# Kernel tuning notes

Measured on AMD Instinct MI355X. Metric: run time of the kernel, lower is better.

Reference implementation:

```python
import jax, jax.numpy as jnp
import numpy as np

T, N = 128, 2048
D_LIN, D_AC, D_IM = 300, 74, 35
H_LIN, H_AC, H_IM = 88, 48, 88
TOT_H = H_LIN + H_AC + H_IM          # 224
ATT_IN = 2 * TOT_H                   # 448 (window_dim=2)
MEM = 128
GAMMA_IN = ATT_IN + MEM              # 576
FINAL = TOT_H + MEM                  # 352
OUT_DIM = 1


def _lin(x, w, b):
    # torch nn.Linear: y = x @ W^T + b, W: [out, in]
    return x @ w.T + b


def _lstm_cell(x, h, c, w_ih, w_hh, b_ih, b_hh):
    # torch nn.LSTMCell gate order: i, f, g, o
    gates = x @ w_ih.T + b_ih + h @ w_hh.T + b_hh
    i, f, g, o = jnp.split(gates, 4, axis=-1)
    c2 = jax.nn.sigmoid(f) * c + jax.nn.sigmoid(i) * jnp.tanh(g)
    h2 = jax.nn.sigmoid(o) * jnp.tanh(c2)
    return h2, c2


def _forward(x_lin, x_ac, x_im, p):
    (W_ih_lin, W_hh_lin, b_ih_lin, b_hh_lin,
     W_ih_ac, W_hh_ac, b_ih_ac, b_hh_ac,
     W_ih_im, W_hh_im, b_ih_im, b_hh_im,
     att1_w1, att1_b1, att1_w2, att1_b2,
     att2_w1, att2_b1, att2_w2, att2_b2,
     g1_w1, g1_b1, g1_w2, g1_b2,
     g2_w1, g2_b1, g2_w2, g2_b2,
     out_w1, out_b1, out_w2, out_b2) = p
    n = x_lin.shape[1]
    z = lambda d: jnp.zeros((n, d), dtype=x_lin.dtype)
    init = (z(H_LIN), z(H_LIN), z(H_AC), z(H_AC), z(H_IM), z(H_IM), z(MEM))

    def step(carry, xs):
        h_l, c_l, h_a, c_a, h_i, c_i, mem = carry
        xl, xa, xi = xs
        nh_l, nc_l = _lstm_cell(xl, h_l, c_l, W_ih_lin, W_hh_lin, b_ih_lin, b_hh_lin)
        nh_a, nc_a = _lstm_cell(xa, h_a, c_a, W_ih_ac, W_hh_ac, b_ih_ac, b_hh_ac)
        nh_i, nc_i = _lstm_cell(xi, h_i, c_i, W_ih_im, W_hh_im, b_ih_im, b_hh_im)
        prev_cs = jnp.concatenate([c_l, c_a, c_i], axis=1)
        new_cs = jnp.concatenate([nc_l, nc_a, nc_i], axis=1)
        c_star = jnp.concatenate([prev_cs, new_cs], axis=1)   # [n, 448]
        attn = jax.nn.softmax(
            _lin(jax.nn.relu(_lin(c_star, att1_w1, att1_b1)), att1_w2, att1_b2), axis=1)
        attended = attn * c_star
        c_hat = jnp.tanh(
            _lin(jax.nn.relu(_lin(attended, att2_w1, att2_b1)), att2_w2, att2_b2))
        both = jnp.concatenate([attended, mem], axis=1)       # [n, 576]
        gamma1 = jax.nn.sigmoid(_lin(jax.nn.relu(_lin(both, g1_w1, g1_b1)), g1_w2, g1_b2))
        gamma2 = jax.nn.sigmoid(_lin(jax.nn.relu(_lin(both, g2_w1, g2_b1)), g2_w2, g2_b2))
        new_mem = gamma1 * mem + gamma2 * c_hat
        return ((nh_l, nc_l, nh_a, nc_a, nh_i, nc_i, new_mem),
                (nh_l, nh_a, nh_i, new_mem))

    _, (hs_l, hs_a, hs_i, mems) = jax.lax.scan(step, init, (x_lin, x_ac, x_im))
    feats = jnp.concatenate([hs_l, hs_a, hs_i, mems], axis=-1)  # [T, n, 352]
    out = _lin(jax.nn.relu(_lin(feats, out_w1, out_b1)), out_w2, out_b2)  # [T, n, 1]
    return jnp.transpose(out, (1, 0, 2))  # [n, T, 1] (torch cats over dim=1)


def setup_inputs() -> dict:
    key = jax.random.key(0)
    ks = iter(jax.random.split(key, 64))

    def rn(shape, s=0.05):
        return (jax.random.normal(next(ks), shape) * s).astype(jnp.float32)

    inp = {
        'x_linguistic': rn((T, N, D_LIN), 1.0),
        'x_acoustic': rn((T, N, D_AC), 1.0),
        'x_image': rn((T, N, D_IM), 1.0),
    }
    for name, din, h in [('lin', D_LIN, H_LIN), ('ac', D_AC, H_AC), ('im', D_IM, H_IM)]:
        inp[f'W_ih_{name}'] = rn((4 * h, din))
        inp[f'W_hh_{name}'] = rn((4 * h, h))
        inp[f'b_ih_{name}'] = rn((4 * h,))
        inp[f'b_hh_{name}'] = rn((4 * h,))
    for nm, hdim, din, dout in [('att1', 128, ATT_IN, ATT_IN),
                                ('att2', 256, ATT_IN, MEM),
                                ('g1', 64, GAMMA_IN, MEM),
                                ('g2', 64, GAMMA_IN, MEM),
                                ('out', 64, FINAL, OUT_DIM)]:
        inp[f'{nm}_w1'] = rn((hdim, din))
        inp[f'{nm}_b1'] = rn((hdim,))
        inp[f'{nm}_w2'] = rn((dout, hdim))
        inp[f'{nm}_b2'] = rn((dout,))
    return inp


def reference(x_linguistic, x_acoustic, x_image,
              W_ih_lin, W_hh_lin, b_ih_lin, b_hh_lin,
              W_ih_ac, W_hh_ac, b_ih_ac, b_hh_ac,
              W_ih_im, W_hh_im, b_ih_im, b_hh_im,
              att1_w1, att1_b1, att1_w2, att1_b2,
              att2_w1, att2_b1, att2_w2, att2_b2,
              g1_w1, g1_b1, g1_w2, g1_b2,
              g2_w1, g2_b1, g2_w2, g2_b2,
              out_w1, out_b1, out_w2, out_b2):
    p = (W_ih_lin, W_hh_lin, b_ih_lin, b_hh_lin,
         W_ih_ac, W_hh_ac, b_ih_ac, b_hh_ac,
         W_ih_im, W_hh_im, b_ih_im, b_hh_im,
         att1_w1, att1_b1, att1_w2, att1_b2,
         att2_w1, att2_b1, att2_w2, att2_b2,
         g1_w1, g1_b1, g1_w2, g1_b2,
         g2_w1, g2_b1, g2_w2, g2_b2,
         out_w1, out_b1, out_w2, out_b2)
    return _forward(x_linguistic, x_acoustic, x_image, p)
```

## Files before the change

kernel.cpp:

```cpp
#include <hip/hip_runtime.h>


#define T_STEPS 128

typedef __attribute__((ext_vector_type(8))) short bf16x8;
typedef __attribute__((ext_vector_type(4))) float f32x4;
typedef __attribute__((ext_vector_type(2))) unsigned long long ull2;

#define MFMA_B16(a,b,c) __builtin_amdgcn_mfma_f32_16x16x32_bf16((a),(b),(c),0,0,0)

__device__ __forceinline__ unsigned short f2b(float v) {
  union { float f; unsigned u; } x; x.f = v;
  unsigned r = x.u + 0x7fffu + ((x.u >> 16) & 1u);
  return (unsigned short)(r >> 16);
}
__device__ __forceinline__ float b2f(unsigned short u) {
  union { unsigned u; float f; } x; x.u = ((unsigned)u) << 16; return x.f;
}
__device__ __forceinline__ float sigm(float x){ return 1.0f/(1.0f + __expf(-x)); }
__device__ __forceinline__ float tanh_(float x){ return 1.0f - 2.0f/(1.0f + __expf(2.0f*x)); }

#define OFF_XL     0
#define OFF_XA     10496
#define OFF_XI     13824
#define OFF_CSTAR  16128
#define OFF_ATT    30720
#define OFF_HID    45312
#define OFF_G1H    53760
#define OFF_G2H    56064
#define OFF_FEATS  58368
#define OFF_BIAS   69888
#define OFF_XP     79368
#define LDS_BYTES  110344

#define BG_LIN 0
#define BG_AC  384
#define BG_IM  576
#define B_A1H  960
#define B_LOG  1088
#define B_A2H  1536
#define B_CHAT 1792
#define B_G1H  1920
#define B_G2H  1984
#define B_GM1  2048
#define B_GM2  2176
#define B_OUTH 2304
#define B_OUT2 2368
#define N_BIAS 2369

#define N_TILES 1718
#define PACK_BYTES ((size_t)N_TILES * 1024)
#define XP_ELEMS ((size_t)262144 * 960)
#define XP_BYTES (XP_ELEMS * 2)

#define LA(off,st,row,kk)  (*(const bf16x8*)(lds + (off) + ((((row)*(st)) + (kk)) << 1)))
#define LB(tile)           (*(const bf16x8*)(packc + (((size_t)(tile)) << 10) + (lane << 4)))
#define STB(off,st,row,col,v) (*(unsigned short*)(lds + (off) + ((((row)*(st)) + (col)) << 1)) = f2b(v))
#define LDB(off,st,row,col)   b2f(*(const unsigned short*)(lds + (off) + ((((row)*(st)) + (col)) << 1)))

struct PP { const float* p[35]; };

__device__ __forceinline__ void vmw(int n) {
  switch (n) {
    case 0: asm volatile("s_waitcnt vmcnt(0)"); break;
    case 1: asm volatile("s_waitcnt vmcnt(1)"); break;
    case 2: asm volatile("s_waitcnt vmcnt(2)"); break;
    case 3: asm volatile("s_waitcnt vmcnt(3)"); break;
    case 4: asm volatile("s_waitcnt vmcnt(4)"); break;
    case 5: asm volatile("s_waitcnt vmcnt(5)"); break;
    case 6: asm volatile("s_waitcnt vmcnt(6)"); break;
    default: asm volatile("s_waitcnt vmcnt(7)"); break;
  }
  __builtin_amdgcn_sched_barrier(0);
}

#define ISSUE_B(dst, tile)                                                   \
  { unsigned off_ = (((unsigned)(tile)) << 10) + ((unsigned)lane << 4);      \
    asm volatile("global_load_dwordx4 %0, %1, %2"                            \
                 : "=v"(dst) : "v"(off_), "s"(packc)); }

template<int NTT, class FT, class FB>
__device__ __forceinline__ void reg_loop(const char* packc, int lane,
                                         FT&& tile_of, FB&& body)
{
  constexpr int D = (NTT < 8) ? NTT : 8;
  bf16x8 b[8];
  #pragma unroll
  for (int i = 0; i < D; ++i) ISSUE_B(b[i], tile_of(i));
  #pragma unroll
  for (int i = 0; i < NTT; ++i) {
    vmw((NTT-1-i) < 7 ? (NTT-1-i) : 7);
    body(i, b[i & 7]);
    __builtin_amdgcn_sched_barrier(0);
    if (i + 8 < NTT) ISSUE_B(b[i & 7], tile_of(i + 8));
  }
}

__device__ __forceinline__ float gate_src(const float* Wih, const float* Whh,
                                          int H, int din, int nksx, int col, int k)
{
  int blk = col >> 6, gate = (col >> 4) & 3, u = col & 15;
  int unit = blk*16 + u;
  if (unit >= H) return 0.f;
  int row = gate*H + unit;
  int xk = nksx*32;
  if (k < xk) return (k < din) ? Wih[row*din + k] : 0.f;
  int kk = k - xk;
  return (kk < H) ? Whh[row*H + kk] : 0.f;
}
__device__ __forceinline__ float gate_h(const float* Whh, int H, int col, int k)
{
  int blk = col >> 6, gate = (col >> 4) & 3, u = col & 15;
  int unit = blk*16 + u;
  if (unit >= H || k >= H) return 0.f;
  return Whh[(gate*H + unit)*H + k];
}
__device__ __forceinline__ float gate_x(const float* Wih, int H, int din, int col, int k)
{
  int blk = col >> 6, gate = (col >> 4) & 3, u = col & 15;
  int unit = blk*16 + u;
  if (unit >= H || k >= din) return 0.f;
  return Wih[(gate*H + unit)*din + k];
}
__device__ __forceinline__ float plain_src(const float* W, int nout, int kdim, int col, int k)
{
  return (col < nout && k < kdim) ? W[col*kdim + k] : 0.f;
}

__global__ __launch_bounds__(256) void pack_kernel(PP P, unsigned short* __restrict__ pack,
                                                   float* __restrict__ bias)
{
  int tid = blockIdx.x*blockDim.x + threadIdx.x;
  int wv = tid >> 6, lane = tid & 63;
  int nw = (gridDim.x*blockDim.x) >> 6;
  int c = lane & 15, kg = lane >> 4;

  for (int tile = wv; tile < N_TILES; tile += nw) {
    unsigned short* dst = pack + ((size_t)tile << 9) + lane*8;
    #pragma unroll
    for (int i = 0; i < 8; ++i) {
      int r = tile; int nt, ks; float v; int kk;
      if (r < 312)       { nt=r/13; ks=r-nt*13; kk=ks*32+kg*8+i; v = gate_src(P.p[3], P.p[4], 88,300,10, nt*16+c, kk); }
      else if (r < 372)  { r-=312; nt=r/5;  ks=r-nt*5;  kk=ks*32+kg*8+i; v = gate_src(P.p[7], P.p[8], 48, 74, 3, nt*16+c, kk); }
      else if (r < 492)  { r-=372; nt=r/5;  ks=r-nt*5;  kk=ks*32+kg*8+i; v = gate_src(P.p[11],P.p[12],88, 35, 2, nt*16+c, kk); }
      else if (r < 604)  { r-=492; nt=r/14; ks=r-nt*14; kk=ks*32+kg*8+i; v = plain_src(P.p[15],128,448, nt*16+c, kk); }
      else if (r < 716)  { r-=604; nt=r/4;  ks=r-nt*4;  kk=ks*32+kg*8+i; v = plain_src(P.p[17],448,128, nt*16+c, kk); }
      else if (r < 940)  { r-=716; nt=r/14; ks=r-nt*14; kk=ks*32+kg*8+i; v = plain_src(P.p[19],256,448, nt*16+c, kk); }
      else if (r < 1004) { r-=940; nt=r/8;  ks=r-nt*8;  kk=ks*32+kg*8+i; v = plain_src(P.p[21],128,256, nt*16+c, kk); }
      else if (r < 1076) { r-=1004; nt=r/18; ks=r-nt*18; kk=ks*32+kg*8+i; v = plain_src(P.p[23], 64,576, nt*16+c, kk); }
      else if (r < 1148) { r-=1076; nt=r/18; ks=r-nt*18; kk=ks*32+kg*8+i; v = plain_src(P.p[27], 64,576, nt*16+c, kk); }
      else if (r < 1164) { r-=1148; nt=r/2;  ks=r-nt*2;  kk=ks*32+kg*8+i; v = plain_src(P.p[25],128, 64, nt*16+c, kk); }
      else if (r < 1180) { r-=1164; nt=r/2;  ks=r-nt*2;  kk=ks*32+kg*8+i; v = plain_src(P.p[29],128, 64, nt*16+c, kk); }
      else if (r < 1224) { r-=1180; nt=r/11; ks=r-nt*11; kk=ks*32+kg*8+i; v = plain_src(P.p[31], 64,352, nt*16+c, kk); }
      else if (r < 1226) { r-=1224; ks=r;    kk=ks*32+kg*8+i; v = plain_src(P.p[33],  1, 64, c, kk); }
      else if (r < 1298) { r-=1226; nt=r/3;  ks=r-nt*3;  kk=ks*32+kg*8+i; v = gate_h(P.p[4], 88, nt*16+c, kk); }
      else if (r < 1322) { r-=1298; nt=r/2;  ks=r-nt*2;  kk=ks*32+kg*8+i; v = gate_h(P.p[8], 48, nt*16+c, kk); }
      else if (r < 1394) { r-=1322; nt=r/3;  ks=r-nt*3;  kk=ks*32+kg*8+i; v = gate_h(P.p[12],88, nt*16+c, kk); }
      else if (r < 1634) { r-=1394; nt=r/10; ks=r-nt*10; kk=ks*32+kg*8+i; v = gate_x(P.p[3], 88,300, nt*16+c, kk); }
      else if (r < 1670) { r-=1634; nt=r/3;  ks=r-nt*3;  kk=ks*32+kg*8+i; v = gate_x(P.p[7], 48, 74, nt*16+c, kk); }
      else               { r-=1670; nt=r/2;  ks=r-nt*2;  kk=ks*32+kg*8+i; v = gate_x(P.p[11],88, 35, nt*16+c, kk); }
      dst[i] = f2b(v);
    }
  }

  int NT = gridDim.x*blockDim.x;
  for (int b = tid; b < N_BIAS; b += NT) {
    float v; int r = b;
    if (r < 384)       { int blk=r>>6, g=(r>>4)&3, u=r&15, un=blk*16+u; v = (un<88) ? P.p[5][g*88+un] + P.p[6][g*88+un]  : 0.f; }
    else if (r < 576)  { r-=384; int blk=r>>6, g=(r>>4)&3, u=r&15, un=blk*16+u; v = (un<48) ? P.p[9][g*48+un] + P.p[10][g*48+un] : 0.f; }
    else if (r < 960)  { r-=576; int blk=r>>6, g=(r>>4)&3, u=r&15, un=blk*16+u; v = (un<88) ? P.p[13][g*88+un]+ P.p[14][g*88+un] : 0.f; }
    else if (r < 1088) v = P.p[16][r-960];
    else if (r < 1536) v = P.p[18][r-1088];
    else if (r < 1792) v = P.p[20][r-1536];
    else if (r < 1920) v = P.p[22][r-1792];
    else if (r < 1984) v = P.p[24][r-1920];
    else if (r < 2048) v = P.p[28][r-1984];
    else if (r < 2176) v = P.p[26][r-2048];
    else if (r < 2304) v = P.p[30][r-2176];
    else if (r < 2368) v = P.p[32][r-2304];
    else               v = P.p[34][0];
    bias[b] = v;
  }
}

__global__ __launch_bounds__(1024) void xproj_kernel(
    const float* __restrict__ xlin, const float* __restrict__ xac,
    const float* __restrict__ xim, const unsigned short* __restrict__ pack,
    unsigned short* __restrict__ xp)
{
  __shared__ alignas(16) char slds[81920];
  const char* packc = (const char*)pack;
  const int tid = threadIdx.x, lane = tid & 63, w = tid >> 6;
  const int rA = lane & 15, gA = lane >> 4;
  const int mt = w & 7, half = w >> 3;
  const size_t m0 = (size_t)blockIdx.x * 128;
  const int mr = mt * 16;

  for (int p = tid; p < 9600; p += 1024) {
    int row = p/75, d = p - row*75;
    float4 v = *(const float4*)(xlin + (m0+row)*300 + d*4);
    unsigned long long u = (unsigned long long)f2b(v.x)
      | ((unsigned long long)f2b(v.y) << 16)
      | ((unsigned long long)f2b(v.z) << 32)
      | ((unsigned long long)f2b(v.w) << 48);
    *(unsigned long long*)(slds + (((size_t)row*320 + d*4) << 1)) = u;
  }
  for (int p = tid; p < 1280; p += 1024) {
    int row = p/10, cc = 300 + 2*(p - row*10);
    *(unsigned*)(slds + (((size_t)row*320 + cc) << 1)) = 0;
  }
  __syncthreads();
  for (int blk = half*3; blk < half*3 + 3; ++blk) {
    #pragma unroll
    for (int q = 0; q < 4; ++q) {
      f32x4 acc = {0.f,0.f,0.f,0.f};
      int nt = blk*4 + q;
      bf16x8 a = *(const bf16x8*)(slds + ((((mr+rA)*320) + gA*8) << 1));
      reg_loop<10>(packc, lane,
        [&](int i){ return 1394 + nt*10 + i; },
        [&](int i, bf16x8 bv){
          acc = MFMA_B16(a, bv, acc);
          if (i + 1 < 10) a = *(const bf16x8*)(slds + ((((mr+rA)*320) + (i+1)*32 + gA*8) << 1));
        });
      #pragma unroll
      for (int j = 0; j < 4; ++j)
        xp[(m0 + mr + gA*4 + j)*960 + blk*64 + q*16 + rA] = f2b(acc[j]);
    }
  }
  __syncthreads();

  for (int p = tid; p < 4736; p += 1024) {
    int row = p/37, d = p - row*37;
    float2 v = *(const float2*)(xac + (m0+row)*74 + d*2);
    unsigned uu = (unsigned)f2b(v.x) | ((unsigned)f2b(v.y) << 16);
    *(unsigned*)(slds + (((size_t)row*96 + d*2) << 1)) = uu;
  }
  for (int p = tid; p < 1408; p += 1024) {
    int row = p/11, cc = 74 + 2*(p - row*11);
    *(unsigned*)(slds + (((size_t)row*96 + cc) << 1)) = 0;
  }
  __syncthreads();
  if (half == 0) {
    for (int blk = 0; blk < 3; ++blk) {
      #pragma unroll
      for (int q = 0; q < 4; ++q) {
        f32x4 acc = {0.f,0.f,0.f,0.f};
        int nt = blk*4 + q;
        bf16x8 a = *(const bf16x8*)(slds + ((((mr+rA)*96) + gA*8) << 1));
        reg_loop<3>(packc, lane,
          [&](int i){ return 1634 + nt*3 + i; },
          [&](int i, bf16x8 bv){
            acc = MFMA_B16(a, bv, acc);
            if (i + 1 < 3) a = *(const bf16x8*)(slds + ((((mr+rA)*96) + (i+1)*32 + gA*8) << 1));
          });
        #pragma unroll
        for (int j = 0; j < 4; ++j)
          xp[(m0 + mr + gA*4 + j)*960 + 384 + blk*64 + q*16 + rA] = f2b(acc[j]);
      }
    }
  }
  __syncthreads();

  for (int p = tid; p < 4480; p += 1024) {
    int row = p/35, d = p - row*35;
    *(unsigned short*)(slds + (((size_t)row*64 + d) << 1)) = f2b(xim[(m0+row)*35 + d]);
  }
  for (int p = tid; p < 3712; p += 1024) {
    int row = p/29, cc = 35 + (p - row*29);
    *(unsigned short*)(slds + (((size_t)row*64 + cc) << 1)) = 0;
  }
  __syncthreads();
  if (half == 1) {
    for (int blk = 0; blk < 6; ++blk) {
      #pragma unroll
      for (int q = 0; q < 4; ++q) {
        f32x4 acc = {0.f,0.f,0.f,0.f};
        int nt = blk*4 + q;
        bf16x8 a = *(const bf16x8*)(slds + ((((mr+rA)*64) + gA*8) << 1));
        reg_loop<2>(packc, lane,
          [&](int i){ return 1670 + nt*2 + i; },
          [&](int i, bf16x8 bv){
            acc = MFMA_B16(a, bv, acc);
            if (i + 1 < 2) a = *(const bf16x8*)(slds + ((((mr+rA)*64) + 32 + gA*8) << 1));
          });
        #pragma unroll
        for (int j = 0; j < 4; ++j)
          xp[(m0 + mr + gA*4 + j)*960 + 576 + blk*64 + q*16 + rA] = f2b(acc[j]);
      }
    }
  }
}

struct GT { int blk, tb, kt, nksx, nks, xoff, xst, hsec, bb, H; };
__device__ __forceinline__ GT gate_task(int tau) {
  GT g;
  if (tau < 6)       { g.blk=tau;   g.tb=0   + g.blk*4*13; g.kt=13; g.nksx=10; g.nks=13; g.xoff=OFF_XL; g.xst=328; g.hsec=0;   g.bb=BG_LIN; g.H=88; }
  else if (tau < 9)  { g.blk=tau-6; g.tb=312 + g.blk*4*5;  g.kt=5;  g.nksx=3;  g.nks=5;  g.xoff=OFF_XA; g.xst=104; g.hsec=88;  g.bb=BG_AC;  g.H=48; }
  else               { g.blk=tau-9; g.tb=372 + g.blk*4*5;  g.kt=5;  g.nksx=2;  g.nks=5;  g.xoff=OFF_XI; g.xst=72;  g.hsec=136; g.bb=BG_IM;  g.H=88; }
  return g;
}

template<int NKSX,int NKS>
__device__ __forceinline__ void gate_reg(f32x4 acc[4], const char* lds, const char* packc,
    int lane, int rA, int gA, int xoff, int xst, int hsec, int tb, int kt)
{
  bf16x8 a = LA(xoff, xst, rA, gA*8);
  reg_loop<NKS*4>(packc, lane,
    [&](int i){ return tb + (i & 3)*kt + (i >> 2); },
    [&](int i, bf16x8 bv){
      int q = i & 3, s = i >> 2;
      acc[q] = MFMA_B16(a, bv, acc[q]);
      if (q == 3 && s + 1 < NKS) {
        int s2 = s + 1;
        a = (s2 < NKSX) ? LA(xoff, xst, rA, s2*32 + gA*8)
                        : LA(OFF_FEATS, 360, rA, hsec + (s2-NKSX)*32 + gA*8);
      }
    });
}

template<int NKS>
__device__ __forceinline__ void gate_reg_h(f32x4 acc[4], const char* lds, const char* packc,
    int lane, int rA, int gA, int hsec, int tb)
{
  bf16x8 a = LA(OFF_FEATS, 360, rA, hsec + gA*8);
  reg_loop<NKS*4>(packc, lane,
    [&](int i){ return tb + (i & 3)*NKS + (i >> 2); },
    [&](int i, bf16x8 bv){
      int q = i & 3, s = i >> 2;
      acc[q] = MFMA_B16(a, bv, acc[q]);
      if (q == 3 && s + 1 < NKS)
        a = LA(OFF_FEATS, 360, rA, hsec + (s+1)*32 + gA*8);
    });
}

__device__ __forceinline__ void stage_x(char* lds, const float* __restrict__ xlin,
    const float* __restrict__ xac, const float* __restrict__ xim, int t, int n0,
    int tid0, int nthr)
{
  const size_t tb = (size_t)t*2048 + n0;
  for (int q = tid0; q < 1200; q += nthr) {
    int row = q/75, d = q - row*75;
    float4 v = *(const float4*)(xlin + (tb+row)*300 + d*4);
    unsigned long long u = (unsigned long long)f2b(v.x)
      | ((unsigned long long)f2b(v.y) << 16)
      | ((unsigned long long)f2b(v.z) << 32)
      | ((unsigned long long)f2b(v.w) << 48);
    *(unsigned long long*)(lds + OFF_XL + (((size_t)row*328 + d*4) << 1)) = u;
  }
  for (int q = tid0; q < 592; q += nthr) {
    int row = q/37, d = q - row*37;
    float2 v = *(const float2*)(xac + (tb+row)*74 + d*2);
    unsigned uu = (unsigned)f2b(v.x) | ((unsigned)f2b(v.y) << 16);
    *(unsigned*)(lds + OFF_XA + (((size_t)row*104 + d*2) << 1)) = uu;
  }
  for (int q = tid0; q < 560; q += nthr) {
    int row = q/35, d = q - row*35;
    *(unsigned short*)(lds + OFF_XI + (((size_t)row*72 + d) << 1)) = f2b(xim[(tb+row)*35 + d]);
  }
}

__device__ __forceinline__ void stage_xp(char* lds, const unsigned short* __restrict__ xp,
                                         int t, int n0, int tid0, int nthr)
{
  const size_t base = ((size_t)t*2048 + n0)*960;
  for (int q = tid0; q < 1920; q += nthr) {
    int row = q/120, ch = q - row*120;
    ull2 v = *(const ull2*)(xp + base + (size_t)row*960 + ch*8);
    *(ull2*)(lds + OFF_XP + (((size_t)row*968 + ch*8) << 1)) = v;
  }
}

template<int XPATH>
__global__ __launch_bounds__(1024) void fused_kernel(
    const float* __restrict__ xlin, const float* __restrict__ xac, const float* __restrict__ xim,
    const unsigned short* __restrict__ pack, const float* __restrict__ biasg,
    const unsigned short* __restrict__ xp, float* __restrict__ out)
{
  __shared__ alignas(16) char lds[LDS_BYTES];
  const char* packc = (const char*)pack;
  const int tid  = threadIdx.x;
  const int lane = tid & 63;
  const int w    = tid >> 6;
  const int rA   = lane & 15;
  const int gA   = lane >> 4;
  const int n0   = blockIdx.x * 16;
  float* biasLds = (float*)(lds + OFF_BIAS);

  for (int i = tid; i < (OFF_BIAS >> 2); i += 1024) ((int*)lds)[i] = 0;
  __syncthreads();
  for (int i = tid; i < N_BIAS; i += 1024) biasLds[i] = biasg[i];
  if (XPATH) stage_xp(lds, xp, 0, n0, tid, 1024);
  else       stage_x(lds, xlin, xac, xim, 0, n0, tid, 1024);
  __syncthreads();

  float cst[4]  = {};
  float mreg[4] = {};

  for (int t = 0; t < T_STEPS; ++t) {
    f32x4 gacc[4];
    if (w == 15) {
      if (t > 0) {
        float bv = biasLds[B_OUT2];
        f32x4 oa0 = {bv,bv,bv,bv};
        bf16x8 as[2], bs[2];
        #pragma unroll
        for (int s = 0; s < 2; ++s) { bs[s] = LB(1224 + s); as[s] = LA(OFF_HID,72, rA, s*32+gA*8); }
        #pragma unroll
        for (int s = 0; s < 2; ++s) oa0 = MFMA_B16(as[s], bs[s], oa0);
        if (rA == 0) {
          #pragma unroll
          for (int j = 0; j < 4; ++j)
            __builtin_nontemporal_store(oa0[j], &out[(size_t)(n0 + gA*4 + j)*T_STEPS + (t-1)]);
        }
      }
    } else if (XPATH) {
      int blk, tb, nks, hsec, bb, cb;
      if (w < 6)      { blk=w;   tb=1226+w*12;      nks=3; hsec=0;   bb=BG_LIN; cb=0   + w*64; }
      else if (w < 9) { blk=w-6; tb=1298+(w-6)*8;   nks=2; hsec=88;  bb=BG_AC;  cb=384 + (w-6)*64; }
      else            { blk=w-9; tb=1322+(w-9)*12;  nks=3; hsec=136; bb=BG_IM;  cb=576 + (w-9)*64; }
      #pragma unroll
      for (int q = 0; q < 4; ++q) {
        float bv = biasLds[bb + blk*64 + q*16 + rA];
        #pragma unroll
        for (int j = 0; j < 4; ++j) {
          int row = gA*4 + j;
          float xv = b2f(*(const unsigned short*)(lds + OFF_XP + (((size_t)row*968 + cb + q*16 + rA) << 1)));
          gacc[q][j] = bv + xv;
        }
      }
      if (nks == 3) gate_reg_h<3>(gacc, lds, packc, lane, rA, gA, hsec, tb);
      else          gate_reg_h<2>(gacc, lds, packc, lane, rA, gA, hsec, tb);
    } else {
      GT g = gate_task(w);
      #pragma unroll
      for (int q = 0; q < 4; ++q) {
        float bv = biasLds[g.bb + g.blk*64 + q*16 + rA];
        gacc[q] = (f32x4){bv,bv,bv,bv};
      }
      if (w < 6)      gate_reg<10,13>(gacc, lds, packc, lane, rA, gA, g.xoff, g.xst, g.hsec, g.tb, g.kt);
      else if (w < 9) gate_reg<3,5>  (gacc, lds, packc, lane, rA, gA, g.xoff, g.xst, g.hsec, g.tb, g.kt);
      else            gate_reg<2,5>  (gacc, lds, packc, lane, rA, gA, g.xoff, g.xst, g.hsec, g.tb, g.kt);
    }
    __syncthreads();

    if (w < 15) {
      GT g = gate_task(w);
      int unit = g.blk*16 + rA;
      if (unit < g.H) {
        #pragma unroll
        for (int j = 0; j < 4; ++j) {
          float iv = sigm (gacc[0][j]);
          float fv = sigm (gacc[1][j]);
          float gv = tanh_(gacc[2][j]);
          float ov = sigm (gacc[3][j]);
          float cp = cst[j];
          float cn = fv*cp + iv*gv;
          float hn = ov*tanh_(cn);
          cst[j] = cn;
          int row = gA*4 + j;
          STB(OFF_CSTAR,456, row, g.hsec + unit,        cp);
          STB(OFF_CSTAR,456, row, 224 + g.hsec + unit,  cn);
          STB(OFF_FEATS,360, row, g.hsec + unit,        hn);
        }
      }
    }
    __syncthreads();

    if (w < 8) {
      int n = w;
      float bv = biasLds[B_A1H + n*16 + rA];
      f32x4 a0v = {bv,bv,bv,bv};
      bf16x8 a = LA(OFF_CSTAR,456, rA, gA*8);
      reg_loop<14>(packc, lane,
        [&](int i){ return 492 + n*14 + i; },
        [&](int i, bf16x8 bv8){
          a0v = MFMA_B16(a, bv8, a0v);
          if (i + 1 < 14) a = LA(OFF_CSTAR,456, rA, (i+1)*32+gA*8);
        });
      #pragma unroll
      for (int j = 0; j < 4; ++j)
        STB(OFF_HID,136, gA*4 + j, n*16 + rA, fmaxf(a0v[j], 0.f));
    }
    __syncthreads();

    {
      float bv1 = biasLds[B_LOG + w*16 + rA];
      if (w < 12) {
        float bv2 = biasLds[B_LOG + (w+16)*16 + rA];
        f32x4 l0 = {bv1,bv1,bv1,bv1}, l1 = {bv2,bv2,bv2,bv2};
        bf16x8 a = LA(OFF_HID,136, rA, gA*8);
        reg_loop<8>(packc, lane,
          [&](int i){ int tau = (i < 4) ? w : (w + 16); return 604 + tau*4 + (i & 3); },
          [&](int i, bf16x8 bv8){
            if (i < 4) l0 = MFMA_B16(a, bv8, l0); else l1 = MFMA_B16(a, bv8, l1);
            if (i + 1 < 8) a = LA(OFF_HID,136, rA, ((i+1)&3)*32+gA*8);
          });
        #pragma unroll
        for (int j = 0; j < 4; ++j) {
          STB(OFF_ATT,456, gA*4 + j, w*16 + rA,      l0[j]);
          STB(OFF_ATT,456, gA*4 + j, (w+16)*16 + rA, l1[j]);
        }
      } else {
        f32x4 l0 = {bv1,bv1,bv1,bv1};
        bf16x8 a = LA(OFF_HID,136, rA, gA*8);
        reg_loop<4>(packc, lane,
          [&](int i){ return 604 + w*4 + i; },
          [&](int i, bf16x8 bv8){
            l0 = MFMA_B16(a, bv8, l0);
            if (i + 1 < 4) a = LA(OFF_HID,136, rA, (i+1)*32+gA*8);
          });
        #pragma unroll
        for (int j = 0; j < 4; ++j)
          STB(OFF_ATT,456, gA*4 + j, w*16 + rA, l0[j]);
      }
    }
    __syncthreads();

    if (w < 8) {
      int row = w*2 + (lane >> 5);
      int cb  = lane & 31;
      float v[14];
      float mx = -3.0e38f;
      #pragma unroll
      for (int q = 0; q < 14; ++q) { v[q] = LDB(OFF_ATT,456,row, cb + 32*q); mx = fmaxf(mx, v[q]); }
      #pragma unroll
      for (int mk = 1; mk < 32; mk <<= 1) mx = fmaxf(mx, __shfl_xor(mx, mk));
      float sm = 0.f;
      #pragma unroll
      for (int q = 0; q < 14; ++q) { v[q] = __expf(v[q] - mx); sm += v[q]; }
      #pragma unroll
      for (int mk = 1; mk < 32; mk <<= 1) sm += __shfl_xor(sm, mk);
      float inv = 1.0f / sm;
      #pragma unroll
      for (int q = 0; q < 14; ++q) {
        int c = cb + 32*q;
        float cs = LDB(OFF_CSTAR,456,row,c);
        STB(OFF_ATT,456,row,c, v[q]*inv*cs);
      }
    } else if (t < T_STEPS-1) {
      if (XPATH) stage_xp(lds, xp, t+1, n0, tid - 512, 512);
      else       stage_x(lds, xlin, xac, xim, t+1, n0, tid - 512, 512);
    }
    __syncthreads();

    if (w >= 8) {
      int nb = (w - 8)*2;
      float b0 = biasLds[B_A2H + nb*16 + rA];
      float b1 = biasLds[B_A2H + (nb+1)*16 + rA];
      f32x4 A0 = {b0,b0,b0,b0}, A1 = {b1,b1,b1,b1};
      bf16x8 a = LA(OFF_ATT,456, rA, gA*8);
      reg_loop<28>(packc, lane,
        [&](int i){ int rr = (i >= 14) ? 1 : 0; int s = i - (rr ? 14 : 0); return 716 + (nb+rr)*14 + s; },
        [&](int i, bf16x8 bv8){
          if (i < 14) A0 = MFMA_B16(a, bv8, A0); else A1 = MFMA_B16(a, bv8, A1);
          if (i + 1 < 28) {
            int ns = (i + 1 < 14) ? (i + 1) : (i + 1 - 14);
            a = LA(OFF_ATT,456, rA, ns*32+gA*8);
          }
        });
      #pragma unroll
      for (int j = 0; j < 4; ++j) {
        STB(OFF_HID,264, gA*4 + j, nb*16 + rA,     fmaxf(A0[j], 0.f));
        STB(OFF_HID,264, gA*4 + j, (nb+1)*16 + rA, fmaxf(A1[j], 0.f));
      }
    } else {
      int which = w >> 2;
      int n = w & 3;
      int tbq = which ? 1076 : 1004;
      int bb  = which ? B_G2H : B_G1H;
      int oo  = which ? OFF_G2H : OFF_G1H;
      float bv = biasLds[bb + n*16 + rA];
      f32x4 A0 = {bv,bv,bv,bv};
      bf16x8 a = LA(OFF_ATT,456, rA, gA*8);
      reg_loop<18>(packc, lane,
        [&](int i){ return tbq + n*18 + i; },
        [&](int i, bf16x8 bv8){
          A0 = MFMA_B16(a, bv8, A0);
          if (i + 1 < 18) {
            a = (i + 1 < 14) ? LA(OFF_ATT,456, rA, (i+1)*32+gA*8)
                             : LA(OFF_FEATS,360, rA, 224 + (i+1-14)*32 + gA*8);
          }
        });
      #pragma unroll
      for (int j = 0; j < 4; ++j)
        STB(oo,72, gA*4 + j, n*16 + rA, fmaxf(A0[j], 0.f));
    }
    __syncthreads();

    if (w < 8) {
      int n = w;
      float bc = biasLds[B_CHAT + n*16 + rA];
      float b1 = biasLds[B_GM1  + n*16 + rA];
      float b2 = biasLds[B_GM2  + n*16 + rA];
      f32x4 cc0={bc,bc,bc,bc};
      f32x4 g10={b1,b1,b1,b1};
      f32x4 g20={b2,b2,b2,b2};
      bf16x8 a = LA(OFF_HID,264, rA, gA*8);
      reg_loop<12>(packc, lane,
        [&](int i){
          if (i < 8)  return 940 + n*8 + i;
          if (i < 10) return 1148 + n*2 + (i - 8);
          return 1164 + n*2 + (i - 10);
        },
        [&](int i, bf16x8 bv8){
          if (i < 8)       cc0 = MFMA_B16(a, bv8, cc0);
          else if (i < 10) g10 = MFMA_B16(a, bv8, g10);
          else             g20 = MFMA_B16(a, bv8, g20);
          if (i + 1 < 8)        a = LA(OFF_HID,264, rA, (i+1)*32+gA*8);
          else if (i + 1 < 10)  a = LA(OFF_G1H,72, rA, (i+1-8)*32+gA*8);
          else if (i + 1 < 12)  a = LA(OFF_G2H,72, rA, (i+1-10)*32+gA*8);
        });
      #pragma unroll
      for (int j = 0; j < 4; ++j) {
        float ch = tanh_(cc0[j]), ga = sigm(g10[j]), gb = sigm(g20[j]);
        float mn = ga*mreg[j] + gb*ch;
        mreg[j] = mn;
        STB(OFF_FEATS,360, gA*4 + j, 224 + n*16 + rA, mn);
      }
    }
    __syncthreads();

    if (w < 4) {
      int n = w;
      float bv = biasLds[B_OUTH + n*16 + rA];
      f32x4 a0v = {bv,bv,bv,bv};
      bf16x8 a = LA(OFF_FEATS,360, rA, gA*8);
      reg_loop<11>(packc, lane,
        [&](int i){ return 1180 + n*11 + i; },
        [&](int i, bf16x8 bv8){
          a0v = MFMA_B16(a, bv8, a0v);
          if (i + 1 < 11) a = LA(OFF_FEATS,360, rA, (i+1)*32+gA*8);
        });
      #pragma unroll
      for (int j = 0; j < 4; ++j)
        STB(OFF_HID,72, gA*4 + j, n*16 + rA, fmaxf(a0v[j], 0.f));
    }
    __syncthreads();
  }

  if (w == 15) {
    float bv = biasLds[B_OUT2];
    f32x4 oa0 = {bv,bv,bv,bv};
    bf16x8 as[2], bs[2];
    #pragma unroll
    for (int s = 0; s < 2; ++s) { bs[s] = LB(1224 + s); as[s] = LA(OFF_HID,72, rA, s*32+gA*8); }
    #pragma unroll
    for (int s = 0; s < 2; ++s) oa0 = MFMA_B16(as[s], bs[s], oa0);
    if (rA == 0) {
      #pragma unroll
      for (int j = 0; j < 4; ++j)
        __builtin_nontemporal_store(oa0[j], &out[(size_t)(n0 + gA*4 + j)*T_STEPS + 127]);
    }
  }
}

extern "C" void kernel_launch(void* const* d_in, const int* in_sizes, int n_in,
                              void* d_out, int out_size, void* d_ws, size_t ws_size,
                              hipStream_t stream) {
  (void)in_sizes; (void)n_in; (void)out_size;
  PP P;
  for (int i = 0; i < 35; ++i) P.p[i] = (const float*)d_in[i];
  unsigned short* pack = (unsigned short*)d_ws;
  float* bias = (float*)((char*)d_ws + PACK_BYTES);
  unsigned short* xp = (unsigned short*)((char*)d_ws + PACK_BYTES + 16384);
  const size_t need = PACK_BYTES + 16384 + XP_BYTES;

  hipLaunchKernelGGL(pack_kernel, dim3(320), dim3(256), 0, stream, P, pack, bias);
  if (ws_size >= need) {
    hipLaunchKernelGGL(xproj_kernel, dim3(2048), dim3(1024), 0, stream,
                       P.p[0], P.p[1], P.p[2], pack, xp);
    hipLaunchKernelGGL(HIP_KERNEL_NAME(fused_kernel<1>), dim3(128), dim3(1024), 0, stream,
                       P.p[0], P.p[1], P.p[2], pack, bias, xp, (float*)d_out);
  } else {
    hipLaunchKernelGGL(HIP_KERNEL_NAME(fused_kernel<0>), dim3(128), dim3(1024), 0, stream,
                       P.p[0], P.p[1], P.p[2], pack, bias, xp, (float*)d_out);
  }
}
```

Before: 4.533 ms.

## Shrink recurrent kernel to 8 waves, pair gate tasks per wave, deepen B prefetch

Cuts the recurrent fused kernel from 16 to 8 waves per block and gives each wave two LSTM gate blocks (twin_gate), merges the attention-hidden and gamma-hidden GEMMs into one 46-tile loop per wave, and raises the in-flight weight prefetch depth from 8 to 16 tiles. The next step's xp staging is now issued as register loads before the softmax and written to LDS afterwards, overlapping the global load with compute. The non-xproj fallback path is removed. The aim is fewer idle waves per barrier and better latency hiding for weight fetches. The cost is more serial MFMA work per wave and higher register pressure.

New measurement: 4.691 ms. 3.5% more time.

```diff
diff --git a/kernel.cpp b/kernel.cpp
--- a/kernel.cpp
+++ b/kernel.cpp
@@ -62,14 +62,22 @@
 
 __device__ __forceinline__ void vmw(int n) {
   switch (n) {
-    case 0: asm volatile("s_waitcnt vmcnt(0)"); break;
-    case 1: asm volatile("s_waitcnt vmcnt(1)"); break;
-    case 2: asm volatile("s_waitcnt vmcnt(2)"); break;
-    case 3: asm volatile("s_waitcnt vmcnt(3)"); break;
-    case 4: asm volatile("s_waitcnt vmcnt(4)"); break;
-    case 5: asm volatile("s_waitcnt vmcnt(5)"); break;
-    case 6: asm volatile("s_waitcnt vmcnt(6)"); break;
-    default: asm volatile("s_waitcnt vmcnt(7)"); break;
+    case 0:  asm volatile("s_waitcnt vmcnt(0)");  break;
+    case 1:  asm volatile("s_waitcnt vmcnt(1)");  break;
+    case 2:  asm volatile("s_waitcnt vmcnt(2)");  break;
+    case 3:  asm volatile("s_waitcnt vmcnt(3)");  break;
+    case 4:  asm volatile("s_waitcnt vmcnt(4)");  break;
+    case 5:  asm volatile("s_waitcnt vmcnt(5)");  break;
+    case 6:  asm volatile("s_waitcnt vmcnt(6)");  break;
+    case 7:  asm volatile("s_waitcnt vmcnt(7)");  break;
+    case 8:  asm volatile("s_waitcnt vmcnt(8)");  break;
+    case 9:  asm volatile("s_waitcnt vmcnt(9)");  break;
+    case 10: asm volatile("s_waitcnt vmcnt(10)"); break;
+    case 11: asm volatile("s_waitcnt vmcnt(11)"); break;
+    case 12: asm volatile("s_waitcnt vmcnt(12)"); break;
+    case 13: asm volatile("s_waitcnt vmcnt(13)"); break;
+    case 14: asm volatile("s_waitcnt vmcnt(14)"); break;
+    default: asm volatile("s_waitcnt vmcnt(15)"); break;
   }
   __builtin_amdgcn_sched_barrier(0);
 }
@@ -83,16 +91,16 @@
 __device__ __forceinline__ void reg_loop(const char* packc, int lane,
                                          FT&& tile_of, FB&& body)
 {
-  constexpr int D = (NTT < 8) ? NTT : 8;
-  bf16x8 b[8];
+  constexpr int D = (NTT < 16) ? NTT : 16;
+  bf16x8 b[16];
   #pragma unroll
   for (int i = 0; i < D; ++i) ISSUE_B(b[i], tile_of(i));
   #pragma unroll
   for (int i = 0; i < NTT; ++i) {
-    vmw((NTT-1-i) < 7 ? (NTT-1-i) : 7);
-    body(i, b[i & 7]);
+    vmw((NTT-1-i) < 15 ? (NTT-1-i) : 15);
+    body(i, b[i & 15]);
     __builtin_amdgcn_sched_barrier(0);
-    if (i + 8 < NTT) ISSUE_B(b[i & 7], tile_of(i + 8));
+    if (i + 16 < NTT) ISSUE_B(b[i & 15], tile_of(i + 16));
   }
 }
 
@@ -291,29 +299,26 @@
   }
 }
 
-struct GT { int blk, tb, kt, nksx, nks, xoff, xst, hsec, bb, H; };
-__device__ __forceinline__ GT gate_task(int tau) {
-  GT g;
-  if (tau < 6)       { g.blk=tau;   g.tb=0   + g.blk*4*13; g.kt=13; g.nksx=10; g.nks=13; g.xoff=OFF_XL; g.xst=328; g.hsec=0;   g.bb=BG_LIN; g.H=88; }
-  else if (tau < 9)  { g.blk=tau-6; g.tb=312 + g.blk*4*5;  g.kt=5;  g.nksx=3;  g.nks=5;  g.xoff=OFF_XA; g.xst=104; g.hsec=88;  g.bb=BG_AC;  g.H=48; }
-  else               { g.blk=tau-9; g.tb=372 + g.blk*4*5;  g.kt=5;  g.nksx=2;  g.nks=5;  g.xoff=OFF_XI; g.xst=72;  g.hsec=136; g.bb=BG_IM;  g.H=88; }
-  return g;
-}
-
-template<int NKSX,int NKS>
-__device__ __forceinline__ void gate_reg(f32x4 acc[4], const char* lds, const char* packc,
-    int lane, int rA, int gA, int xoff, int xst, int hsec, int tb, int kt)
-{
-  bf16x8 a = LA(xoff, xst, rA, gA*8);
-  reg_loop<NKS*4>(packc, lane,
-    [&](int i){ return tb + (i & 3)*kt + (i >> 2); },
+template<int NA,int NB>
+__device__ __forceinline__ void twin_gate(f32x4 aA[4], f32x4 aB[4], const char* lds,
+    const char* packc, int lane, int rA, int gA,
+    int tbA, int hsA, int tbB, int hsB)
+{
+  bf16x8 a;
+  reg_loop<(NA+NB)*4>(packc, lane,
+    [&](int i){
+      if (i < NA*4) { int j = i;        return tbA + (j&3)*NA + (j>>2); }
+      else          { int j = i - NA*4; return tbB + (j&3)*NB + (j>>2); }
+    },
     [&](int i, bf16x8 bv){
-      int q = i & 3, s = i >> 2;
-      acc[q] = MFMA_B16(a, bv, acc[q]);
-      if (q == 3 && s + 1 < NKS) {
-        int s2 = s + 1;
-        a = (s2 < NKSX) ? LA(xoff, xst, rA, s2*32 + gA*8)
-                        : LA(OFF_FEATS, 360, rA, hsec + (s2-NKSX)*32 + gA*8);
+      if (i < NA*4) {
+        int q = i & 3, s = i >> 2;
+        if (q == 0) a = LA(OFF_FEATS,360, rA, hsA + s*32 + gA*8);
+        aA[q] = MFMA_B16(a, bv, aA[q]);
+      } else {
+        int j = i - NA*4, q = j & 3, s = j >> 2;
+        if (q == 0) a = LA(OFF_FEATS,360, rA, hsB + s*32 + gA*8);
+        aB[q] = MFMA_B16(a, bv, aB[q]);
       }
     });
 }
@@ -322,57 +327,17 @@
 __device__ __forceinline__ void gate_reg_h(f32x4 acc[4], const char* lds, const char* packc,
     int lane, int rA, int gA, int hsec, int tb)
 {
-  bf16x8 a = LA(OFF_FEATS, 360, rA, hsec + gA*8);
+  bf16x8 a;
   reg_loop<NKS*4>(packc, lane,
     [&](int i){ return tb + (i & 3)*NKS + (i >> 2); },
     [&](int i, bf16x8 bv){
       int q = i & 3, s = i >> 2;
+      if (q == 0) a = LA(OFF_FEATS, 360, rA, hsec + s*32 + gA*8);
       acc[q] = MFMA_B16(a, bv, acc[q]);
-      if (q == 3 && s + 1 < NKS)
-        a = LA(OFF_FEATS, 360, rA, hsec + (s+1)*32 + gA*8);
     });
 }
 
-__device__ __forceinline__ void stage_x(char* lds, const float* __restrict__ xlin,
-    const float* __restrict__ xac, const float* __restrict__ xim, int t, int n0,
-    int tid0, int nthr)
-{
-  const size_t tb = (size_t)t*2048 + n0;
-  for (int q = tid0; q < 1200; q += nthr) {
-    int row = q/75, d = q - row*75;
-    float4 v = *(const float4*)(xlin + (tb+row)*300 + d*4);
-    unsigned long long u = (unsigned long long)f2b(v.x)
-      | ((unsigned long long)f2b(v.y) << 16)
-      | ((unsigned long long)f2b(v.z) << 32)
-      | ((unsigned long long)f2b(v.w) << 48);
-    *(unsigned long long*)(lds + OFF_XL + (((size_t)row*328 + d*4) << 1)) = u;
-  }
-  for (int q = tid0; q < 592; q += nthr) {
-    int row = q/37, d = q - row*37;
-    float2 v = *(const float2*)(xac + (tb+row)*74 + d*2);
-    unsigned uu = (unsigned)f2b(v.x) | ((unsigned)f2b(v.y) << 16);
-    *(unsigned*)(lds + OFF_XA + (((size_t)row*104 + d*2) << 1)) = uu;
-  }
-  for (int q = tid0; q < 560; q += nthr) {
-    int row = q/35, d = q - row*35;
-    *(unsigned short*)(lds + OFF_XI + (((size_t)row*72 + d) << 1)) = f2b(xim[(tb+row)*35 + d]);
-  }
-}
-
-__device__ __forceinline__ void stage_xp(char* lds, const unsigned short* __restrict__ xp,
-                                         int t, int n0, int tid0, int nthr)
-{
-  const size_t base = ((size_t)t*2048 + n0)*960;
-  for (int q = tid0; q < 1920; q += nthr) {
-    int row = q/120, ch = q - row*120;
-    ull2 v = *(const ull2*)(xp + base + (size_t)row*960 + ch*8);
-    *(ull2*)(lds + OFF_XP + (((size_t)row*968 + ch*8) << 1)) = v;
-  }
-}
-
-template<int XPATH>
-__global__ __launch_bounds__(1024) void fused_kernel(
-    const float* __restrict__ xlin, const float* __restrict__ xac, const float* __restrict__ xim,
+__global__ __launch_bounds__(512, 2) void fused_kernel(
     const unsigned short* __restrict__ pack, const float* __restrict__ biasg,
     const unsigned short* __restrict__ xp, float* __restrict__ out)
 {
@@ -386,87 +351,116 @@
   const int n0   = blockIdx.x * 16;
   float* biasLds = (float*)(lds + OFF_BIAS);
 
-  for (int i = tid; i < (OFF_BIAS >> 2); i += 1024) ((int*)lds)[i] = 0;
+  for (int i = tid; i < (OFF_BIAS >> 2); i += 512) ((int*)lds)[i] = 0;
   __syncthreads();
-  for (int i = tid; i < N_BIAS; i += 1024) biasLds[i] = biasg[i];
-  if (XPATH) stage_xp(lds, xp, 0, n0, tid, 1024);
-  else       stage_x(lds, xlin, xac, xim, 0, n0, tid, 1024);
+  for (int i = tid; i < N_BIAS; i += 512) biasLds[i] = biasg[i];
+  {
+    const size_t base0 = ((size_t)n0) * 960;
+    for (int q = tid; q < 1920; q += 512) {
+      int row = q/120, ch = q - row*120;
+      ull2 v = __builtin_nontemporal_load((const ull2*)(xp + base0 + (size_t)row*960 + ch*8));
+      *(ull2*)(lds + OFF_XP + (((size_t)row*968 + ch*8) << 1)) = v;
+    }
+  }
   __syncthreads();
 
-  float cst[4]  = {};
+  float cstA[4] = {}, cstB[4] = {};
   float mreg[4] = {};
 
+  int tbA, hsA, cbA, HA, blkA;
+  if (w < 6)      { tbA = 1226 + w*12; hsA = 0;  cbA = w*64;  HA = 88; blkA = w; }
+  else if (w==6)  { tbA = 1298;        hsA = 88; cbA = 384;   HA = 48; blkA = 0; }
+  else            { tbA = 1306;        hsA = 88; cbA = 448;   HA = 48; blkA = 1; }
+  int tbB, hsB, cbB, HB, blkB;
+  if (w == 0)     { tbB = 1314;            hsB = 88;  cbB = 512;          HB = 48; blkB = 2; }
+  else            { tbB = 1322 + (w-1)*12; hsB = 136; cbB = 576+(w-1)*64; HB = 88; blkB = w-1; }
+
   for (int t = 0; t < T_STEPS; ++t) {
-    f32x4 gacc[4];
-    if (w == 15) {
-      if (t > 0) {
-        float bv = biasLds[B_OUT2];
-        f32x4 oa0 = {bv,bv,bv,bv};
-        bf16x8 as[2], bs[2];
-        #pragma unroll
-        for (int s = 0; s < 2; ++s) { bs[s] = LB(1224 + s); as[s] = LA(OFF_HID,72, rA, s*32+gA*8); }
-        #pragma unroll
-        for (int s = 0; s < 2; ++s) oa0 = MFMA_B16(as[s], bs[s], oa0);
-        if (rA == 0) {
-          #pragma unroll
-          for (int j = 0; j < 4; ++j)
-            __builtin_nontemporal_store(oa0[j], &out[(size_t)(n0 + gA*4 + j)*T_STEPS + (t-1)]);
-        }
-      }
-    } else if (XPATH) {
-      int blk, tb, nks, hsec, bb, cb;
-      if (w < 6)      { blk=w;   tb=1226+w*12;      nks=3; hsec=0;   bb=BG_LIN; cb=0   + w*64; }
-      else if (w < 9) { blk=w-6; tb=1298+(w-6)*8;   nks=2; hsec=88;  bb=BG_AC;  cb=384 + (w-6)*64; }
-      else            { blk=w-9; tb=1322+(w-9)*12;  nks=3; hsec=136; bb=BG_IM;  cb=576 + (w-9)*64; }
+    f32x4 gaccA[4], gaccB[4];
+    {
       #pragma unroll
       for (int q = 0; q < 4; ++q) {
-        float bv = biasLds[bb + blk*64 + q*16 + rA];
+        float bvA = biasLds[cbA + q*16 + rA];
         #pragma unroll
         for (int j = 0; j < 4; ++j) {
           int row = gA*4 + j;
-          float xv = b2f(*(const unsigned short*)(lds + OFF_XP + (((size_t)row*968 + cb + q*16 + rA) << 1)));
-          gacc[q][j] = bv + xv;
+          gaccA[q][j] = bvA + b2f(*(const unsigned short*)(lds + OFF_XP + (((size_t)row*968 + cbA + q*16 + rA) << 1)));
         }
-      }
-      if (nks == 3) gate_reg_h<3>(gacc, lds, packc, lane, rA, gA, hsec, tb);
-      else          gate_reg_h<2>(gacc, lds, packc, lane, rA, gA, hsec, tb);
-    } else {
-      GT g = gate_task(w);
-      #pragma unroll
-      for (int q = 0; q < 4; ++q) {
-        float bv = biasLds[g.bb + g.blk*64 + q*16 + rA];
-        gacc[q] = (f32x4){bv,bv,bv,bv};
-      }
-      if (w < 6)      gate_reg<10,13>(gacc, lds, packc, lane, rA, gA, g.xoff, g.xst, g.hsec, g.tb, g.kt);
-      else if (w < 9) gate_reg<3,5>  (gacc, lds, packc, lane, rA, gA, g.xoff, g.xst, g.hsec, g.tb, g.kt);
-      else            gate_reg<2,5>  (gacc, lds, packc, lane, rA, gA, g.xoff, g.xst, g.hsec, g.tb, g.kt);
-    }
-    __syncthreads();
-
-    if (w < 15) {
-      GT g = gate_task(w);
-      int unit = g.blk*16 + rA;
-      if (unit < g.H) {
+        if (w < 7) {
+          float bvB = biasLds[cbB + q*16 + rA];
+          #pragma unroll
+          for (int j = 0; j < 4; ++j) {
+            int row = gA*4 + j;
+            gaccB[q][j] = bvB + b2f(*(const unsigned short*)(lds + OFF_XP + (((size_t)row*968 + cbB + q*16 + rA) << 1)));
+          }
+        }
+      }
+      if (w == 0)      twin_gate<3,2>(gaccA, gaccB, lds, packc, lane, rA, gA, tbA, hsA, tbB, hsB);
+      else if (w < 6)  twin_gate<3,3>(gaccA, gaccB, lds, packc, lane, rA, gA, tbA, hsA, tbB, hsB);
+      else if (w == 6) twin_gate<2,3>(gaccA, gaccB, lds, packc, lane, rA, gA, tbA, hsA, tbB, hsB);
+      else {
+        gate_reg_h<2>(gaccA, lds, packc, lane, rA, gA, hsA, tbA);
+        if (t > 0) {
+          float bv = biasLds[B_OUT2];
+          f32x4 oa0 = {bv,bv,bv,bv};
+          bf16x8 as[2], bs[2];
+          #pragma unroll
+          for (int s = 0; s < 2; ++s) { bs[s] = LB(1224 + s); as[s] = LA(OFF_HID,72, rA, s*32+gA*8); }
+          #pragma unroll
+          for (int s = 0; s < 2; ++s) oa0 = MFMA_B16(as[s], bs[s], oa0);
+          if (rA == 0) {
+            #pragma unroll
+            for (int j = 0; j < 4; ++j)
+              __builtin_nontemporal_store(oa0[j], &out[(size_t)(n0 + gA*4 + j)*T_STEPS + (t-1)]);
+          }
+        }
+      }
+    }
+    __syncthreads();
+
+    {
+      int unitA = blkA*16 + rA;
+      if (unitA < HA) {
         #pragma unroll
         for (int j = 0; j < 4; ++j) {
-          float iv = sigm (gacc[0][j]);
-          float fv = sigm (gacc[1][j]);
-          float gv = tanh_(gacc[2][j]);
-          float ov = sigm (gacc[3][j]);
-          float cp = cst[j];
+          float iv = sigm (gaccA[0][j]);
+          float fv = sigm (gaccA[1][j]);
+          float gv = tanh_(gaccA[2][j]);
+          float ov = sigm (gaccA[3][j]);
+          float cp = cstA[j];
           float cn = fv*cp + iv*gv;
           float hn = ov*tanh_(cn);
-          cst[j] = cn;
+          cstA[j] = cn;
           int row = gA*4 + j;
-          STB(OFF_CSTAR,456, row, g.hsec + unit,        cp);
-          STB(OFF_CSTAR,456, row, 224 + g.hsec + unit,  cn);
-          STB(OFF_FEATS,360, row, g.hsec + unit,        hn);
+          STB(OFF_CSTAR,456, row, hsA + unitA,        cp);
+          STB(OFF_CSTAR,456, row, 224 + hsA + unitA,  cn);
+          STB(OFF_FEATS,360, row, hsA + unitA,        hn);
         }
       }
-    }
-    __syncthreads();
-
-    if (w < 8) {
+      if (w < 7) {
+        int unitB = blkB*16 + rA;
+        if (unitB < HB) {
+          #pragma unroll
+          for (int j = 0; j < 4; ++j) {
+            float iv = sigm (gaccB[0][j]);
+            float fv = sigm (gaccB[1][j]);
+            float gv = tanh_(gaccB[2][j]);
+            float ov = sigm (gaccB[3][j]);
+            float cp = cstB[j];
+            float cn = fv*cp + iv*gv;
+            float hn = ov*tanh_(cn);
+            cstB[j] = cn;
+            int row = gA*4 + j;
+            STB(OFF_CSTAR,456, row, hsB + unitB,        cp);
+            STB(OFF_CSTAR,456, row, 224 + hsB + unitB,  cn);
+            STB(OFF_FEATS,360, row, hsB + unitB,        hn);
+          }
+        }
+      }
+    }
+    __syncthreads();
+
+    {
       int n = w;
       float bv = biasLds[B_A1H + n*16 + rA];
       f32x4 a0v = {bv,bv,bv,bv};
@@ -484,39 +478,51 @@
     __syncthreads();
 
     {
-      float bv1 = biasLds[B_LOG + w*16 + rA];
-      if (w < 12) {
-        float bv2 = biasLds[B_LOG + (w+16)*16 + rA];
-        f32x4 l0 = {bv1,bv1,bv1,bv1}, l1 = {bv2,bv2,bv2,bv2};
-        bf16x8 a = LA(OFF_HID,136, rA, gA*8);
-        reg_loop<8>(packc, lane,
-          [&](int i){ int tau = (i < 4) ? w : (w + 16); return 604 + tau*4 + (i & 3); },
-          [&](int i, bf16x8 bv8){
-            if (i < 4) l0 = MFMA_B16(a, bv8, l0); else l1 = MFMA_B16(a, bv8, l1);
-            if (i + 1 < 8) a = LA(OFF_HID,136, rA, ((i+1)&3)*32+gA*8);
-          });
-        #pragma unroll
-        for (int j = 0; j < 4; ++j) {
-          STB(OFF_ATT,456, gA*4 + j, w*16 + rA,      l0[j]);
-          STB(OFF_ATT,456, gA*4 + j, (w+16)*16 + rA, l1[j]);
+      bf16x8 a4[4];
+      #pragma unroll
+      for (int s = 0; s < 4; ++s) a4[s] = LA(OFF_HID,136, rA, s*32+gA*8);
+      f32x4 l[4];
+      #pragma unroll
+      for (int k = 0; k < 4; ++k) {
+        float bv = biasLds[B_LOG + (w + 8*k)*16 + rA];
+        l[k] = (f32x4){bv,bv,bv,bv};
+      }
+      if (w < 4) {
+        reg_loop<16>(packc, lane,
+          [&](int i){ return 604 + (w + 8*(i>>2))*4 + (i&3); },
+          [&](int i, bf16x8 bv8){ l[i>>2] = MFMA_B16(a4[i&3], bv8, l[i>>2]); });
+        #pragma unroll
+        for (int k = 0; k < 4; ++k)
+          #pragma unroll
+          for (int j = 0; j < 4; ++j)
+            STB(OFF_ATT,456, gA*4 + j, (w + 8*k)*16 + rA, l[k][j]);
+      } else {
+        reg_loop<12>(packc, lane,
+          [&](int i){ return 604 + (w + 8*(i>>2))*4 + (i&3); },
+          [&](int i, bf16x8 bv8){ l[i>>2] = MFMA_B16(a4[i&3], bv8, l[i>>2]); });
+        #pragma unroll
+        for (int k = 0; k < 3; ++k)
+          #pragma unroll
+          for (int j = 0; j < 4; ++j)
+            STB(OFF_ATT,456, gA*4 + j, (w + 8*k)*16 + rA, l[k][j]);
+      }
+    }
+    __syncthreads();
+
+    {
+      ull2 xr[4];
+      const bool do_stage = (t < T_STEPS-1);
+      const size_t base = ((size_t)(t+1)*2048 + n0)*960;
+      if (do_stage) {
+        #pragma unroll
+        for (int k = 0; k < 4; ++k) {
+          int q = tid + k*512;
+          if (q < 1920) {
+            int row = q/120, ch = q - row*120;
+            xr[k] = __builtin_nontemporal_load((const ull2*)(xp + base + (size_t)row*960 + ch*8));
+          }
         }
-      } else {
-        f32x4 l0 = {bv1,bv1,bv1,bv1};
-        bf16x8 a = LA(OFF_HID,136, rA, gA*8);
-        reg_loop<4>(packc, lane,
-          [&](int i){ return 604 + w*4 + i; },
-          [&](int i, bf16x8 bv8){
-            l0 = MFMA_B16(a, bv8, l0);
-            if (i + 1 < 4) a = LA(OFF_HID,136, rA, (i+1)*32+gA*8);
-          });
-        #pragma unroll
-        for (int j = 0; j < 4; ++j)
-          STB(OFF_ATT,456, gA*4 + j, w*16 + rA, l0[j]);
-      }
-    }
-    __syncthreads();
-
-    if (w < 8) {
+      }
       int row = w*2 + (lane >> 5);
       int cb  = lane & 31;
       float v[14];
@@ -537,57 +543,62 @@
         float cs = LDB(OFF_CSTAR,456,row,c);
         STB(OFF_ATT,456,row,c, v[q]*inv*cs);
       }
-    } else if (t < T_STEPS-1) {
-      if (XPATH) stage_xp(lds, xp, t+1, n0, tid - 512, 512);
-      else       stage_x(lds, xlin, xac, xim, t+1, n0, tid - 512, 512);
-    }
-    __syncthreads();
-
-    if (w >= 8) {
-      int nb = (w - 8)*2;
+      if (do_stage) {
+        asm volatile("s_waitcnt vmcnt(0)");
+        __builtin_amdgcn_sched_barrier(0);
+        #pragma unroll
+        for (int k = 0; k < 4; ++k) {
+          int q = tid + k*512;
+          if (q < 1920) {
+            int row2 = q/120, ch = q - row2*120;
+            *(ull2*)(lds + OFF_XP + (((size_t)row2*968 + ch*8) << 1)) = xr[k];
+          }
+        }
+      }
+    }
+    __syncthreads();
+
+    {
+      int nb = w*2;
+      int which = w >> 2, n = w & 3;
+      int tbq = which ? 1076 : 1004;
+      int bb  = which ? B_G2H : B_G1H;
+      int oo  = which ? OFF_G2H : OFF_G1H;
       float b0 = biasLds[B_A2H + nb*16 + rA];
       float b1 = biasLds[B_A2H + (nb+1)*16 + rA];
-      f32x4 A0 = {b0,b0,b0,b0}, A1 = {b1,b1,b1,b1};
-      bf16x8 a = LA(OFF_ATT,456, rA, gA*8);
-      reg_loop<28>(packc, lane,
-        [&](int i){ int rr = (i >= 14) ? 1 : 0; int s = i - (rr ? 14 : 0); return 716 + (nb+rr)*14 + s; },
+      float bg = biasLds[bb + n*16 + rA];
+      f32x4 A0 = {b0,b0,b0,b0}, A1 = {b1,b1,b1,b1}, G = {bg,bg,bg,bg};
+      reg_loop<46>(packc, lane,
+        [&](int i){
+          if (i < 14) return 716 + nb*14 + i;
+          if (i < 28) return 716 + (nb+1)*14 + (i-14);
+          return tbq + n*18 + (i-28);
+        },
         [&](int i, bf16x8 bv8){
-          if (i < 14) A0 = MFMA_B16(a, bv8, A0); else A1 = MFMA_B16(a, bv8, A1);
-          if (i + 1 < 28) {
-            int ns = (i + 1 < 14) ? (i + 1) : (i + 1 - 14);
-            a = LA(OFF_ATT,456, rA, ns*32+gA*8);
+          if (i < 14) {
+            bf16x8 a = LA(OFF_ATT,456, rA, i*32+gA*8);
+            A0 = MFMA_B16(a, bv8, A0);
+          } else if (i < 28) {
+            int s = i - 14;
+            bf16x8 a = LA(OFF_ATT,456, rA, s*32+gA*8);
+            A1 = MFMA_B16(a, bv8, A1);
+          } else {
+            int s = i - 28;
+            bf16x8 a = (s < 14) ? LA(OFF_ATT,456, rA, s*32+gA*8)
+                                : LA(OFF_FEATS,360, rA, 224 + (s-14)*32 + gA*8);
+            G = MFMA_B16(a, bv8, G);
           }
         });
       #pragma unroll
       for (int j = 0; j < 4; ++j) {
         STB(OFF_HID,264, gA*4 + j, nb*16 + rA,     fmaxf(A0[j], 0.f));
         STB(OFF_HID,264, gA*4 + j, (nb+1)*16 + rA, fmaxf(A1[j], 0.f));
-      }
-    } else {
-      int which = w >> 2;
-      int n = w & 3;
-      int tbq = which ? 1076 : 1004;
-      int bb  = which ? B_G2H : B_G1H;
-      int oo  = which ? OFF_G2H : OFF_G1H;
-      float bv = biasLds[bb + n*16 + rA];
-      f32x4 A0 = {bv,bv,bv,bv};
-      bf16x8 a = LA(OFF_ATT,456, rA, gA*8);
-      reg_loop<18>(packc, lane,
-        [&](int i){ return tbq + n*18 + i; },
-        [&](int i, bf16x8 bv8){
-          A0 = MFMA_B16(a, bv8, A0);
-          if (i + 1 < 18) {
-            a = (i + 1 < 14) ? LA(OFF_ATT,456, rA, (i+1)*32+gA*8)
-                             : LA(OFF_FEATS,360, rA, 224 + (i+1-14)*32 + gA*8);
-          }
-        });
-      #pragma unroll
-      for (int j = 0; j < 4; ++j)
-        STB(oo,72, gA*4 + j, n*16 + rA, fmaxf(A0[j], 0.f));
-    }
-    __syncthreads();
-
-    if (w < 8) {
+        STB(oo,72,       gA*4 + j, n*16 + rA,      fmaxf(G[j],  0.f));
+      }
+    }
+    __syncthreads();
+
+    {
       int n = w;
       float bc = biasLds[B_CHAT + n*16 + rA];
       float b1 = biasLds[B_GM1  + n*16 + rA];
@@ -607,8 +618,10 @@
           else if (i < 10) g10 = MFMA_B16(a, bv8, g10);
           else             g20 = MFMA_B16(a, bv8, g20);
           if (i + 1 < 8)        a = LA(OFF_HID,264, rA, (i+1)*32+gA*8);
-          else if (i + 1 < 10)  a = LA(OFF_G1H,72, rA, (i+1-8)*32+gA*8);
-          else if (i + 1 < 12)  a = LA(OFF_G2H,72, rA, (i+1-10)*32+gA*8);
+          else if (i + 1 == 8)  a = LA(OFF_G1H,72, rA, gA*8);
+          else if (i + 1 == 9)  a = LA(OFF_G1H,72, rA, 32+gA*8);
+          else if (i + 1 == 10) a = LA(OFF_G2H,72, rA, gA*8);
+          else if (i + 1 == 11) a = LA(OFF_G2H,72, rA, 32+gA*8);
         });
       #pragma unroll
       for (int j = 0; j < 4; ++j) {
@@ -638,7 +651,7 @@
     __syncthreads();
   }
 
-  if (w == 15) {
+  if (w == 7) {
     float bv = biasLds[B_OUT2];
     f32x4 oa0 = {bv,bv,bv,bv};
     bf16x8 as[2], bs[2];
@@ -657,22 +670,16 @@
 extern "C" void kernel_launch(void* const* d_in, const int* in_sizes, int n_in,
                               void* d_out, int out_size, void* d_ws, size_t ws_size,
                               hipStream_t stream) {
-  (void)in_sizes; (void)n_in; (void)out_size;
+  (void)in_sizes; (void)n_in; (void)out_size; (void)ws_size;
   PP P;
   for (int i = 0; i < 35; ++i) P.p[i] = (const float*)d_in[i];
   unsigned short* pack = (unsigned short*)d_ws;
   float* bias = (float*)((char*)d_ws + PACK_BYTES);
   unsigned short* xp = (unsigned short*)((char*)d_ws + PACK_BYTES + 16384);
-  const size_t need = PACK_BYTES + 16384 + XP_BYTES;
 
   hipLaunchKernelGGL(pack_kernel, dim3(320), dim3(256), 0, stream, P, pack, bias);
-  if (ws_size >= need) {
-    hipLaunchKernelGGL(xproj_kernel, dim3(2048), dim3(1024), 0, stream,
-                       P.p[0], P.p[1], P.p[2], pack, xp);
-    hipLaunchKernelGGL(HIP_KERNEL_NAME(fused_kernel<1>), dim3(128), dim3(1024), 0, stream,
-                       P.p[0], P.p[1], P.p[2], pack, bias, xp, (float*)d_out);
-  } else {
-    hipLaunchKernelGGL(HIP_KERNEL_NAME(fused_kernel<0>), dim3(128), dim3(1024), 0, stream,
-                       P.p[0], P.p[1], P.p[2], pack, bias, xp, (float*)d_out);
-  }
-}
+  hipLaunchKernelGGL(xproj_kernel, dim3(2048), dim3(1024), 0, stream,
+                     P.p[0], P.p[1], P.p[2], pack, xp);
+  hipLaunchKernelGGL(fused_kernel, dim3(128), dim3(512), 0, stream,
+                     pack, bias, xp, (float*)d_out);
+}
```
